# Kernel tuning notes

Hardware: AMD Instinct MI355X
Metric: run time of the kernel (lower is better)

The kernel has to match this reference:

```python
import jax, jax.numpy as jnp
import numpy as np

N_NODES = 50000
N_EDGES = 800000
D_IN, D_HID, D_OUT = 16, 64, 16
N_BLOCKS = 4


def setup_inputs() -> dict:
    key = jax.random.key(0)
    ks = jax.random.split(key, 12)
    s = 0.05  # small init scale to keep sum-aggregation over 4 blocks stable
    return {
        "x": jax.random.normal(ks[0], (N_NODES, D_IN), jnp.float32),
        "lframes": jax.random.normal(ks[1], (N_NODES, 4, 4), jnp.float32),
        "edge_index": jax.random.randint(ks[2], (2, N_EDGES), 0, N_NODES, jnp.int64),
        "lin_in_w": jax.random.normal(ks[3], (D_IN, D_HID), jnp.float32) * s,
        "lin_in_b": jnp.zeros((D_HID,), jnp.float32),
        # per-block mlp1: Linear(2D->D), ReLU, Linear(D->D), ReLU, Linear(D->D)
        "w0": jax.random.normal(ks[4], (N_BLOCKS, 2 * D_HID, D_HID), jnp.float32) * s,
        "b0": jnp.zeros((N_BLOCKS, D_HID), jnp.float32),
        "w1": jax.random.normal(ks[5], (N_BLOCKS, D_HID, D_HID), jnp.float32) * s,
        "b1": jnp.zeros((N_BLOCKS, D_HID), jnp.float32),
        "w2": jax.random.normal(ks[6], (N_BLOCKS, D_HID, D_HID), jnp.float32) * s,
        "b2": jnp.zeros((N_BLOCKS, D_HID), jnp.float32),
        "lin_out_w": jax.random.normal(ks[7], (D_HID, D_OUT), jnp.float32) * s,
        "lin_out_b": jnp.zeros((D_OUT,), jnp.float32),
    }


def reference(x, lframes, edge_index, lin_in_w, lin_in_b,
              w0, b0, w1, b1, w2, b2, lin_out_w, lin_out_b):
    src = edge_index[0]  # x_j (source / neighbor)
    dst = edge_index[1]  # x_i (target / aggregation node)
    h = x @ lin_in_w + lin_in_b  # [N, D]
    for k in range(N_BLOCKS):
        # message: cat((x_j, x_i)) -> mlp1 ; mlp2 is Identity (num_layers_mlp2=0)
        m = jnp.concatenate((h[src], h[dst]), axis=-1)  # [E, 2D]
        m = jax.nn.relu(m @ w0[k] + b0[k])
        m = jax.nn.relu(m @ w1[k] + b1[k])
        m = m @ w2[k] + b2[k]  # [E, D]
        # aggregate: scatter-add at target node
        h = jax.ops.segment_sum(m, dst, num_segments=N_NODES)
    return h @ lin_out_w + lin_out_b  # [N, D_OUT]
```

## Files before the change

kernel.cpp:

```cpp
#include <hip/hip_runtime.h>
#include <hip/hip_bf16.h>

#define N_NODES 50000
#define N_EDGES 800000
#define D_IN    16
#define D_HID   64
#define D_OUT   16
#define NCHUNK  ((N_NODES + 255) / 256)
#define TMAX    100352
#define GE8     ((N_EDGES / 8 + 255) / 256)
#define GH      ((N_NODES * D_HID + 255) / 256)
#define SCAP    48
#define NSLOTV  (N_NODES * SCAP / 8)

typedef __hip_bfloat16 bf16;
typedef _Float16 f16;
typedef _Float16 f16x8 __attribute__((ext_vector_type(8)));
typedef _Float16 f16x4 __attribute__((ext_vector_type(4)));
typedef float    f32x4 __attribute__((ext_vector_type(4)));
typedef _Float16 f16x8a __attribute__((ext_vector_type(8), may_alias));
typedef _Float16 f16x4a __attribute__((ext_vector_type(4), may_alias));
typedef int      i32x4 __attribute__((ext_vector_type(4)));
typedef unsigned short u16x8a __attribute__((ext_vector_type(8), may_alias));
typedef float    f32x4a __attribute__((ext_vector_type(4), may_alias));

__device__ __forceinline__ float b2f(bf16 v) { return __bfloat162float(v); }
__device__ __forceinline__ float bfb(unsigned short u) {
    union { unsigned u; float f; } z; z.u = (unsigned)u << 16; return z.f;
}
__device__ __forceinline__ int clampn(int v) {
    return v < 0 ? 0 : (v >= N_NODES ? N_NODES - 1 : v);
}
__device__ __forceinline__ float rdf(const void* p, long i, int isbf) {
    return isbf ? b2f(((const bf16*)p)[i]) : ((const float*)p)[i];
}
__device__ __forceinline__ f16x8 relu8(f16x8 v) {
#pragma unroll
    for (int j = 0; j < 8; j++) v[j] = v[j] > (f16)0 ? v[j] : (f16)0;
    return v;
}
__device__ __forceinline__ f16x4 relu4(f16x4 v) {
#pragma unroll
    for (int j = 0; j < 4; j++) v[j] = v[j] > (f16)0 ? v[j] : (f16)0;
    return v;
}
__device__ __forceinline__ int sbase(int m) {
    return (m & 0xFFFFF) * SCAP + ((m >> 25) & 3) * 16;
}

__global__ __launch_bounds__(256) void k_detect(const unsigned short* __restrict__ xw,
                                                const int* __restrict__ ei,
                                                int* __restrict__ flags,
                                                int* __restrict__ cursor,
                                                unsigned short* __restrict__ slots,
                                                unsigned short* __restrict__ psrc_us)
{
    int gtid = blockIdx.x * 256 + threadIdx.x;
    if (gtid < N_NODES) cursor[gtid] = 0;
    const int dpat = (int)0xC350C350;
    const i32x4 fillv = {dpat, dpat, dpat, dpat};
#pragma unroll
    for (int k = 0; k < 6; k++) {
        int q = k * (NCHUNK * 256) + gtid;
        if (q < NSLOTV) ((i32x4*)slots)[q] = fillv;
    }
    if (blockIdx.x == 0 && threadIdx.x < 64)
        psrc_us[(size_t)N_NODES * 64 + threadIdx.x] = 0xFC00u;
    if (blockIdx.x == 0 && threadIdx.x == 0) {
        int inband = 0;
        for (int j = 0; j < 256; j++) {
            unsigned short w = xw[2 * j];
            int e = (w >> 7) & 0xFF;
            if ((w & 0x7FFF) == 0 || (e >= 100 && e <= 140)) inband++;
        }
        flags[0] = (inband >= 192) ? 1 : 0;
        int z = 1;
        for (int j = 1; j < 128; j += 2) z &= (ei[j] == 0) ? 1 : 0;
        flags[1] = z;
    }
}

__global__ __launch_bounds__(256) void k_prep(const int* __restrict__ flags,
                                              const void* __restrict__ gw0,
                                              const void* __restrict__ gw1,
                                              const void* __restrict__ gw2,
                                              f16* __restrict__ wfrag,
                                              const int* __restrict__ eidx,
                                              int* __restrict__ cursor,
                                              unsigned short* __restrict__ slots,
                                              const void* __restrict__ x,
                                              const void* __restrict__ liw,
                                              const void* __restrict__ lib,
                                              float* __restrict__ h,
                                              const void* __restrict__ gb1,
                                              const void* __restrict__ gb2,
                                              float* __restrict__ cpad)
{
    const int isbf = flags[0];
    const int bid = blockIdx.x;
    if (bid < 32) {
        int idx = bid * 256 + threadIdx.x;
        int kb = idx >> 11, rem = idx & 2047;
        int slot = rem >> 6, lane = rem & 63;
        int lm = lane & 15, quad = lane >> 4;
        f16* outp = wfrag + (long)idx * 8;
        if (slot < 16) {
            int c = slot >> 2, q = slot & 3;
            long base = (long)kb * 2 * D_HID * D_HID;
#pragma unroll
            for (int j = 0; j < 8; j++)
                outp[j] = (f16)rdf(gw0, base + (long)(c * 32 + quad * 8 + j) * 64 + q * 16 + lm, isbf);
        } else {
            const void* gw = (slot < 24) ? gw1 : gw2;
            int s = (slot < 24) ? slot - 16 : slot - 24;
            int c = s >> 2, q = s & 3;
            long base = (long)kb * D_HID * D_HID;
#pragma unroll
            for (int j = 0; j < 8; j++)
                outp[j] = (f16)rdf(gw, base + (long)(c * 32 + quad * 8 + j) * 64 + q * 16 + lm, isbf);
        }
    } else if (bid < 32 + GE8) {
        int base = ((bid - 32) * 256 + threadIdx.x) * 8;
        if (base >= N_EDGES) return;
        const int strd = flags[1] ? 2 : 1;
        const long dbase = flags[1] ? (long)(2 * N_EDGES) : (long)N_EDGES;
        int d[8], s[8], pos[8], cnt = min(8, N_EDGES - base);
#pragma unroll
        for (int j = 0; j < 8; j++)
            if (j < cnt) {
                d[j] = clampn(eidx[dbase + (long)(base + j) * strd]);
                s[j] = clampn(eidx[(long)(base + j) * strd]);
            }
#pragma unroll
        for (int j = 0; j < 8; j++)
            if (j < cnt) pos[j] = atomicAdd(&cursor[d[j]], 1);
#pragma unroll
        for (int j = 0; j < 8; j++)
            if (j < cnt && pos[j] < SCAP)
                slots[d[j] * SCAP + pos[j]] = (unsigned short)s[j];
    } else if (bid < 32 + GE8 + GH) {
        int idx = (bid - 32 - GE8) * 256 + threadIdx.x;
        if (idx >= N_NODES * D_HID) return;
        int n = idx >> 6, c = idx & 63;
        float acc, wr[16], xr[16];
        if (isbf) {
            const unsigned short* xp = (const unsigned short*)x + (long)n * 16;
            u16x8a x0 = *(const u16x8a*)xp, x1 = *(const u16x8a*)(xp + 8);
#pragma unroll
            for (int i = 0; i < 8; i++) { xr[i] = bfb(x0[i]); xr[8 + i] = bfb(x1[i]); }
            const unsigned short* wq = (const unsigned short*)liw;
#pragma unroll
            for (int i = 0; i < 16; i++) wr[i] = bfb(wq[i * 64 + c]);
            acc = bfb(((const unsigned short*)lib)[c]);
        } else {
            const float* xp = (const float*)x + (long)n * 16;
#pragma unroll
            for (int q = 0; q < 4; q++) {
                f32x4a v = *(const f32x4a*)(xp + q * 4);
#pragma unroll
                for (int j = 0; j < 4; j++) xr[q * 4 + j] = v[j];
            }
            const float* wq = (const float*)liw;
#pragma unroll
            for (int i = 0; i < 16; i++) wr[i] = wq[i * 64 + c];
            acc = ((const float*)lib)[c];
        }
#pragma unroll
        for (int i = 0; i < 16; i++) acc += xr[i] * wr[i];
        h[idx] = acc;
    } else {
        int t = threadIdx.x;
        int k = t >> 6, j = t & 63;
        float acc = rdf(gb2, (long)k * 64 + j, isbf);
        for (int i = 0; i < 64; i++) {
            float zi = (float)(f16)fmaxf(rdf(gb1, (long)k * 64 + i, isbf), 0.f);
            float wi = (float)(f16)rdf(gw2, (long)k * 4096 + (long)i * 64 + j, isbf);
            acc += zi * wi;
        }
        cpad[k * 64 + j] = acc;
    }
}

__global__ __launch_bounds__(256) void k_scan1(const int* __restrict__ deg,
                                               int* __restrict__ bsum_t)
{
    __shared__ int rt[256];
    const int t = threadIdx.x;
    int i = blockIdx.x * 256 + t;
    int v = (i < N_NODES) ? deg[i] : 0;
    rt[t] = min((v + 15) >> 4, 3);
    __syncthreads();
    for (int d = 128; d > 0; d >>= 1) {
        if (t < d) rt[t] += rt[t + d];
        __syncthreads();
    }
    if (t == 0) bsum_t[blockIdx.x] = rt[0];
}

__global__ __launch_bounds__(256) void k_scan2(const int* __restrict__ bsum_t,
                                               int* __restrict__ boff_t,
                                               int* __restrict__ tot_t)
{
    __shared__ int st_[256];
    const int t = threadIdx.x;
    st_[t] = (t < NCHUNK) ? bsum_t[t] : 0;
    __syncthreads();
    for (int d = 1; d < 256; d <<= 1) {
        int vt = (t >= d) ? st_[t - d] : 0;
        __syncthreads();
        st_[t] += vt;
        __syncthreads();
    }
    if (t < NCHUNK) boff_t[t] = (t == 0) ? 0 : st_[t - 1];
    if (t == NCHUNK - 1) tot_t[0] = st_[t];
}

__global__ __launch_bounds__(256) void k_scan3(const int* __restrict__ deg,
                                               const int* __restrict__ boff_t,
                                               int* __restrict__ toff,
                                               int* __restrict__ tmeta)
{
    __shared__ int st_[256];
    const int t = threadIdx.x;
    int i = blockIdx.x * 256 + t;
    int v = (i < N_NODES) ? deg[i] : 0;
    int w = min((v + 15) >> 4, 3);
    st_[t] = w;
    __syncthreads();
    for (int d = 1; d < 256; d <<= 1) {
        int ut = (t >= d) ? st_[t - d] : 0;
        __syncthreads();
        st_[t] += ut;
        __syncthreads();
    }
    if (i < N_NODES) {
        int exT = boff_t[blockIdx.x] + st_[t] - w;
        toff[i] = exT;
        for (int j = 0; j < w; j++)
            tmeta[exT + j] = i | (min(16, v - 16 * j) << 20) | (j << 25);
    }
}

#define HP_ST 72

__global__ __launch_bounds__(256) void k_proj(
    const int* __restrict__ flags, float* hio,
    const f16* __restrict__ wfrag, const void* __restrict__ gb0,
    const int* __restrict__ deg,
    f16* __restrict__ psrc, f16* __restrict__ pdst, int kblk)
{
    __shared__ f16 hL_s[4][16 * HP_ST];

    const int tid  = threadIdx.x;
    const int isbf = flags[0];
    const int wv = tid >> 6, ln = tid & 63;
    const int lm = ln & 15, quad = ln >> 4;
    f16* hL = hL_s[wv];

    const int g = blockIdx.x * 4 + wv;
    if (g >= N_NODES / 16) return;
    const int n0 = g * 16;

    const f16* wb = wfrag + (long)kblk * 32 * 64 * 8;

#pragma unroll
    for (int i = 0; i < 16; i++) {
        int idx = i * 64 + ln;
        hL[(idx >> 6) * HP_ST + (idx & 63)] = (f16)hio[(long)n0 * 64 + idx];
    }
#pragma unroll
    for (int i = 0; i < 16; i++)
        if (deg[n0 + i] == 0) hio[(long)(n0 + i) * 64 + ln] = 0.f;

    f16x8 a[2];
#pragma unroll
    for (int c = 0; c < 2; c++)
        a[c] = *(const f16x8a*)&hL[lm * HP_ST + c * 32 + quad * 8];

    f32x4 accS[4], accD[4];
#pragma unroll
    for (int q = 0; q < 4; q++) {
        float bd = rdf(gb0, (long)kblk * 64 + q * 16 + lm, isbf);
        accS[q] = (f32x4){0.f, 0.f, 0.f, 0.f};
        accD[q] = (f32x4){bd, bd, bd, bd};
    }
#pragma unroll
    for (int c = 0; c < 2; c++)
#pragma unroll
        for (int q = 0; q < 4; q++) {
            f16x8 bs = *(const f16x8a*)&wb[(((c + 0) * 4 + q) * 64 + ln) * 8];
            f16x8 bd = *(const f16x8a*)&wb[(((c + 2) * 4 + q) * 64 + ln) * 8];
            accS[q] = __builtin_amdgcn_mfma_f32_16x16x32_f16(a[c], bs, accS[q], 0, 0, 0);
            accD[q] = __builtin_amdgcn_mfma_f32_16x16x32_f16(a[c], bd, accD[q], 0, 0, 0);
        }
#pragma unroll
    for (int q = 0; q < 4; q++)
#pragma unroll
        for (int r = 0; r < 4; r++) {
            long o = (long)(n0 + quad * 4 + r) * 64 + q * 16 + lm;
            psrc[o] = (f16)accS[q][r];
            pdst[o] = (f16)accD[q][r];
        }
}

#define Y_ST 72

__global__ __launch_bounds__(256) void k_edge_tile(
    const int* __restrict__ flags,
    const unsigned short* __restrict__ slots, const int* __restrict__ tmeta,
    const int* __restrict__ toff,
    const f16* __restrict__ psrc, const f16* __restrict__ pdst,
    float* __restrict__ hout,
    const f16* __restrict__ wfrag, const void* __restrict__ gb1,
    const void* __restrict__ gb2, const float* __restrict__ cpad, int kblk)
{
    __shared__ f16 y_s[4][16 * Y_ST];
    __shared__ float b1L[64], b2L[64], cpL[64];

    const int tid  = threadIdx.x;
    const int isbf = flags[0];
    const int wv = tid >> 6, ln = tid & 63;
    const int lm = ln & 15, quad = ln >> 4;
    const int sub = ln & 7, eh = ln >> 3;
    f16* y = y_s[wv];

    if (tid < 64)       b1L[tid]       = rdf(gb1, (long)kblk * 64 + tid, isbf);
    else if (tid < 128) b2L[tid - 64]  = rdf(gb2, (long)kblk * 64 + (tid - 64), isbf);
    else if (tid < 192) cpL[tid - 128] = cpad[kblk * 64 + (tid - 128)];
    __syncthreads();

    const f16* wb = wfrag + (long)kblk * 32 * 64 * 8;
    f16x8 bw1[2][4], bw2[2][4];
#pragma unroll
    for (int c = 0; c < 2; c++)
#pragma unroll
        for (int q = 0; q < 4; q++) {
            bw1[c][q] = *(const f16x8a*)&wb[((16 + c * 4 + q) * 64 + ln) * 8];
            bw2[c][q] = *(const f16x8a*)&wb[((24 + c * 4 + q) * 64 + ln) * 8];
        }

    const int T  = toff[N_NODES];
    const int W  = gridDim.x * 4;
    const int gw = blockIdx.x * 4 + wv;
    int t0 = (int)((long)gw * T / W);
    int t1 = (int)((long)(gw + 1) * T / W);
    if (t0 > 0)
        while (t0 < T && (tmeta[t0] & 0xFFFFF) == (tmeta[t0 - 1] & 0xFFFFF)) t0++;
    if (t1 > 0)
        while (t1 < T && (tmeta[t1] & 0xFFFFF) == (tmeta[t1 - 1] & 0xFFFFF)) t1++;
    if (t0 >= t1) return;

    int mA = tmeta[t0];
    int mB = tmeta[min(t0 + 1, T - 1)];
    int mC = tmeta[min(t0 + 2, T - 1)];
    int bA = sbase(mA), bB = sbase(mB);
    int sAa = slots[bA + eh], sAb = slots[bA + 8 + eh];
    int sBa = slots[bB + eh], sBb = slots[bB + 8 + eh];
    f16x8 psAa = *(const f16x8a*)&psrc[(long)sAa * 64 + sub * 8];
    f16x8 psAb = *(const f16x8a*)&psrc[(long)sAb * 64 + sub * 8];
    f16x8 pdA  = *(const f16x8a*)&pdst[(long)(mA & 0xFFFFF) * 64 + sub * 8];

    f32x4 accv[4];
#pragma unroll
    for (int q = 0; q < 4; q++) accv[q] = (f32x4){0.f, 0.f, 0.f, 0.f};

    for (int tt = t0; tt < t1; ++tt) {
        const int mD = tmeta[min(tt + 3, T - 1)];
        const int bC = sbase(mC);
        const int sCa = slots[bC + eh], sCb = slots[bC + 8 + eh];
        f16x8 psBa = *(const f16x8a*)&psrc[(long)sBa * 64 + sub * 8];
        f16x8 psBb = *(const f16x8a*)&psrc[(long)sBb * 64 + sub * 8];
        f16x8 pdB  = *(const f16x8a*)&pdst[(long)(mB & 0xFFFFF) * 64 + sub * 8];

        *(f16x8a*)&y[eh * Y_ST + sub * 8]       = relu8(psAa + pdA);
        *(f16x8a*)&y[(8 + eh) * Y_ST + sub * 8] = relu8(psAb + pdA);

        f16x8 a1[2];
        a1[0] = *(const f16x8a*)&y[lm * Y_ST + quad * 8];
        a1[1] = *(const f16x8a*)&y[lm * Y_ST + 32 + quad * 8];
        f32x4 acc1[4];
#pragma unroll
        for (int q = 0; q < 4; q++)
            acc1[q] = *(const f32x4a*)&b1L[q * 16 + quad * 4];
#pragma unroll
        for (int c = 0; c < 2; c++)
#pragma unroll
            for (int q = 0; q < 4; q++)
                acc1[q] = __builtin_amdgcn_mfma_f32_16x16x32_f16(bw1[c][q], a1[c], acc1[q], 0, 0, 0);
#pragma unroll
        for (int q = 0; q < 4; q++) {
            f16x4 pk = { (f16)acc1[q][0], (f16)acc1[q][1],
                         (f16)acc1[q][2], (f16)acc1[q][3] };
            *(f16x4a*)&y[lm * Y_ST + q * 16 + quad * 4] = relu4(pk);
        }

        f16x8 a2[2];
        a2[0] = *(const f16x8a*)&y[lm * Y_ST + quad * 8];
        a2[1] = *(const f16x8a*)&y[lm * Y_ST + 32 + quad * 8];
#pragma unroll
        for (int c = 0; c < 2; c++)
#pragma unroll
            for (int q = 0; q < 4; q++)
                accv[q] = __builtin_amdgcn_mfma_f32_16x16x32_f16(a2[c], bw2[c][q], accv[q], 0, 0, 0);

        const int curn = mA & 0xFFFFF;
        const int nxt  = (tt + 1 < t1) ? (mB & 0xFFFFF) : -1;
        if (nxt != curn) {
            const float npad = (float)(16 - ((mA >> 20) & 31));
            const float nt16 = (float)((((mA >> 25) & 3) + 1) * 16);
#pragma unroll
            for (int q = 0; q < 4; q++) {
                float v = accv[q][0] + accv[q][1] + accv[q][2] + accv[q][3];
                v += __shfl_xor(v, 16, 64);
                v += __shfl_xor(v, 32, 64);
                if (quad == 0) {
                    const int f = q * 16 + lm;
                    hout[(long)curn * 64 + f] = v + nt16 * b2L[f] - npad * cpL[f];
                }
                accv[q] = (f32x4){0.f, 0.f, 0.f, 0.f};
            }
        }

        mA = mB; mB = mC; mC = mD;
        sBa = sCa; sBb = sCb;
        psAa = psBa; psAb = psBb; pdA = pdB;
    }
}

__global__ __launch_bounds__(256) void k_lin_out(const int* __restrict__ flags,
                                                 const float* __restrict__ h,
                                                 const void* __restrict__ w,
                                                 const void* __restrict__ b,
                                                 float* __restrict__ out)
{
    __shared__ float wl[D_HID * D_OUT];
    __shared__ float bl[D_OUT];
    const int isbf = flags[0];
    const int t = threadIdx.x;
    for (int k = t; k < D_HID * D_OUT; k += 256) wl[k] = rdf(w, k, isbf);
    if (t < D_OUT) bl[t] = rdf(b, t, isbf);
    __syncthreads();

    int idx = blockIdx.x * 256 + t;
    if (idx >= N_NODES * D_OUT) return;
    int n = idx >> 4, c = idx & 15;
    const float* hr = h + (long)n * D_HID;
    float acc = bl[c];
#pragma unroll
    for (int i = 0; i < 16; i++) {
        f32x4a v = *(const f32x4a*)(hr + i * 4);
        acc += v[0] * wl[(i * 4 + 0) * 16 + c] + v[1] * wl[(i * 4 + 1) * 16 + c]
             + v[2] * wl[(i * 4 + 2) * 16 + c] + v[3] * wl[(i * 4 + 3) * 16 + c];
    }
    out[idx] = acc;
}

extern "C" void kernel_launch(void* const* d_in, const int* in_sizes, int n_in,
                              void* d_out, int out_size, void* d_ws, size_t ws_size,
                              hipStream_t stream)
{
    const void* x    = d_in[0];
    const int*  ei   = (const int*)d_in[2];
    const void* liw  = d_in[3];
    const void* lib  = d_in[4];
    const void* w0   = d_in[5];
    const void* b0   = d_in[6];
    const void* w1   = d_in[7];
    const void* b1   = d_in[8];
    const void* w2   = d_in[9];
    const void* b2   = d_in[10];
    const void* low  = d_in[11];
    const void* lob  = d_in[12];
    float* out = (float*)d_out;

    char* wp = (char*)d_ws;
    int*   flags  = (int*)wp;                 wp += 256;
    float* hA     = (float*)wp;               wp += (size_t)N_NODES * D_HID * 4;
    f16*   Psrc   = (f16*)wp;                 wp += ((size_t)N_NODES + 1) * D_HID * 2;
    f16*   Pdst   = (f16*)wp;                 wp += (size_t)N_NODES * D_HID * 2;
    f16*   wfrag  = (f16*)wp;                 wp += (size_t)4 * 32 * 64 * 8 * 2;
    float* cpad   = (float*)wp;               wp += (size_t)4 * 64 * 4;
    int*   cursor = (int*)wp;                 wp += (size_t)N_NODES * 4;
    int*   bsum_t = (int*)wp;                 wp += 256 * 4;
    int*   boff_t = (int*)wp;                 wp += 256 * 4;
    int*   tmeta  = (int*)wp;                 wp += (size_t)TMAX * 4;
    unsigned short* slots = (unsigned short*)wp; wp += (size_t)N_NODES * SCAP * 2;
    int*   toff   = (int*)wp;

    k_detect<<<NCHUNK, 256, 0, stream>>>((const unsigned short*)x, ei, flags,
                                         cursor, slots, (unsigned short*)Psrc);
    k_prep<<<32 + GE8 + GH + 1, 256, 0, stream>>>(flags, w0, w1, w2, wfrag,
                                                  ei, cursor, slots,
                                                  x, liw, lib, hA, b1, b2, cpad);

    k_scan1<<<NCHUNK, 256, 0, stream>>>(cursor, bsum_t);
    k_scan2<<<1, 256, 0, stream>>>(bsum_t, boff_t, toff + N_NODES);
    k_scan3<<<NCHUNK, 256, 0, stream>>>(cursor, boff_t, toff, tmeta);

    for (int k = 0; k < 4; k++) {
        k_proj<<<(N_NODES / 16 + 3) / 4, 256, 0, stream>>>(flags, hA, wfrag, b0,
                                                           cursor, Psrc, Pdst, k);
        k_edge_tile<<<2048, 256, 0, stream>>>(flags, slots, tmeta, toff,
                                              Psrc, Pdst, hA, wfrag, b1, b2,
                                              cpad, k);
    }

    k_lin_out<<<(N_NODES * D_OUT + 255) / 256, 256, 0, stream>>>(flags, hA, low, lob, out);
}
```

Before: 397.0 us.

## Replace global per-node atomics with two-level bucketed CSR build in LDS

Edge slot construction is now two-level. Edges are first binned into coarse buckets of 512 destination nodes using block-local LDS counters and one global atomic per bucket. A new per-bucket kernel then builds the per-node slot lists in shared memory and writes them out along with the degrees and tile counts. This replaces per-edge global atomics on cursors, the full global slot pre-fill and the separate scan1 kernel. In exchange it adds an intermediate bucket buffer with a fixed capacity per bucket (BCAP) that could overflow on skewed inputs, and the bucket kernel runs on only 98 blocks.

```diff
diff --git a/kernel.cpp b/kernel.cpp
--- a/kernel.cpp
+++ b/kernel.cpp
@@ -11,7 +11,8 @@
 #define GE8     ((N_EDGES / 8 + 255) / 256)
 #define GH      ((N_NODES * D_HID + 255) / 256)
 #define SCAP    48
-#define NSLOTV  (N_NODES * SCAP / 8)
+#define NB      98
+#define BCAP    12288
 
 typedef __hip_bfloat16 bf16;
 typedef _Float16 f16;
@@ -20,7 +21,6 @@
 typedef float    f32x4 __attribute__((ext_vector_type(4)));
 typedef _Float16 f16x8a __attribute__((ext_vector_type(8), may_alias));
 typedef _Float16 f16x4a __attribute__((ext_vector_type(4), may_alias));
-typedef int      i32x4 __attribute__((ext_vector_type(4)));
 typedef unsigned short u16x8a __attribute__((ext_vector_type(8), may_alias));
 typedef float    f32x4a __attribute__((ext_vector_type(4), may_alias));
 
@@ -51,22 +51,13 @@
 __global__ __launch_bounds__(256) void k_detect(const unsigned short* __restrict__ xw,
                                                 const int* __restrict__ ei,
                                                 int* __restrict__ flags,
-                                                int* __restrict__ cursor,
-                                                unsigned short* __restrict__ slots,
+                                                int* __restrict__ gbcnt,
                                                 unsigned short* __restrict__ psrc_us)
 {
-    int gtid = blockIdx.x * 256 + threadIdx.x;
-    if (gtid < N_NODES) cursor[gtid] = 0;
-    const int dpat = (int)0xC350C350;
-    const i32x4 fillv = {dpat, dpat, dpat, dpat};
-#pragma unroll
-    for (int k = 0; k < 6; k++) {
-        int q = k * (NCHUNK * 256) + gtid;
-        if (q < NSLOTV) ((i32x4*)slots)[q] = fillv;
-    }
-    if (blockIdx.x == 0 && threadIdx.x < 64)
-        psrc_us[(size_t)N_NODES * 64 + threadIdx.x] = 0xFC00u;
-    if (blockIdx.x == 0 && threadIdx.x == 0) {
+    const int t = threadIdx.x;
+    if (t < 64) psrc_us[(size_t)N_NODES * 64 + t] = 0xFC00u;
+    if (t < NB) gbcnt[t] = 0;
+    if (t == 0) {
         int inband = 0;
         for (int j = 0; j < 256; j++) {
             unsigned short w = xw[2 * j];
@@ -86,8 +77,8 @@
                                               const void* __restrict__ gw2,
                                               f16* __restrict__ wfrag,
                                               const int* __restrict__ eidx,
-                                              int* __restrict__ cursor,
-                                              unsigned short* __restrict__ slots,
+                                              int* __restrict__ gbcnt,
+                                              unsigned int* __restrict__ gbuckets,
                                               const void* __restrict__ x,
                                               const void* __restrict__ liw,
                                               const void* __restrict__ lib,
@@ -120,24 +111,37 @@
                 outp[j] = (f16)rdf(gw, base + (long)(c * 32 + quad * 8 + j) * 64 + q * 16 + lm, isbf);
         }
     } else if (bid < 32 + GE8) {
-        int base = ((bid - 32) * 256 + threadIdx.x) * 8;
-        if (base >= N_EDGES) return;
+        __shared__ int cnt[NB], base[NB];
+        const int t = threadIdx.x;
+        for (int k = t; k < NB; k += 256) cnt[k] = 0;
+        __syncthreads();
+        const int ebase = ((bid - 32) * 256 + t) * 8;
+        const int cntv = (ebase < N_EDGES) ? min(8, N_EDGES - ebase) : 0;
         const int strd = flags[1] ? 2 : 1;
         const long dbase = flags[1] ? (long)(2 * N_EDGES) : (long)N_EDGES;
-        int d[8], s[8], pos[8], cnt = min(8, N_EDGES - base);
+        int d[8], s[8], r[8];
 #pragma unroll
         for (int j = 0; j < 8; j++)
-            if (j < cnt) {
-                d[j] = clampn(eidx[dbase + (long)(base + j) * strd]);
-                s[j] = clampn(eidx[(long)(base + j) * strd]);
+            if (j < cntv) {
+                d[j] = clampn(eidx[dbase + (long)(ebase + j) * strd]);
+                s[j] = clampn(eidx[(long)(ebase + j) * strd]);
             }
 #pragma unroll
         for (int j = 0; j < 8; j++)
-            if (j < cnt) pos[j] = atomicAdd(&cursor[d[j]], 1);
+            if (j < cntv) r[j] = atomicAdd(&cnt[d[j] >> 9], 1);
+        __syncthreads();
+        for (int k = t; k < NB; k += 256)
+            base[k] = cnt[k] ? atomicAdd(&gbcnt[k], cnt[k]) : 0;
+        __syncthreads();
 #pragma unroll
         for (int j = 0; j < 8; j++)
-            if (j < cnt && pos[j] < SCAP)
-                slots[d[j] * SCAP + pos[j]] = (unsigned short)s[j];
+            if (j < cntv) {
+                int b = d[j] >> 9;
+                int p = base[b] + r[j];
+                if (p < BCAP)
+                    gbuckets[(size_t)b * BCAP + p] =
+                        ((unsigned)(d[j] & 511) << 16) | (unsigned)s[j];
+            }
     } else if (bid < 32 + GE8 + GH) {
         int idx = (bid - 32 - GE8) * 256 + threadIdx.x;
         if (idx >= N_NODES * D_HID) return;
@@ -181,20 +185,50 @@
     }
 }
 
-__global__ __launch_bounds__(256) void k_scan1(const int* __restrict__ deg,
-                                               int* __restrict__ bsum_t)
-{
-    __shared__ int rt[256];
-    const int t = threadIdx.x;
-    int i = blockIdx.x * 256 + t;
-    int v = (i < N_NODES) ? deg[i] : 0;
-    rt[t] = min((v + 15) >> 4, 3);
+__global__ __launch_bounds__(256) void k_bucket(const int* __restrict__ gbcnt,
+                                                const unsigned int* __restrict__ gbuckets,
+                                                unsigned short* __restrict__ slots,
+                                                int* __restrict__ deg,
+                                                int* __restrict__ bsum_t)
+{
+    __shared__ unsigned short sl[512 * SCAP];
+    __shared__ int cur[512];
+    __shared__ int red[256];
+    const int t = threadIdx.x, b = blockIdx.x;
+
+    for (int k = t; k < 512; k += 256) cur[k] = 0;
+    unsigned int* sl32 = (unsigned int*)sl;
+    for (int k = t; k < 512 * SCAP / 2; k += 256) sl32[k] = 0xC350C350u;
     __syncthreads();
-    for (int d = 128; d > 0; d >>= 1) {
-        if (t < d) rt[t] += rt[t + d];
-        __syncthreads();
-    }
-    if (t == 0) bsum_t[blockIdx.x] = rt[0];
+
+    const int ne = min(gbcnt[b], BCAP);
+    const unsigned int* eb = gbuckets + (size_t)b * BCAP;
+    for (int k = t; k < ne; k += 256) {
+        unsigned int rec = eb[k];
+        int n = rec >> 16;
+        int pos = atomicAdd(&cur[n], 1);
+        if (pos < SCAP) sl[n * SCAP + pos] = (unsigned short)(rec & 0xFFFFu);
+    }
+    __syncthreads();
+
+    const int n0 = b * 512;
+    const int nn = min(512, N_NODES - n0);
+    unsigned int* gs32 = (unsigned int*)slots;
+    for (int k = t; k < nn * SCAP / 2; k += 256)
+        gs32[(size_t)n0 * SCAP / 2 + k] = sl32[k];
+    for (int half = 0; half < 2; half++) {
+        int n = half * 256 + t;
+        int dv = (n < nn) ? cur[n] : 0;
+        if (n < nn) deg[n0 + n] = dv;
+        red[t] = min((dv + 15) >> 4, 3);
+        __syncthreads();
+        for (int d2 = 128; d2 > 0; d2 >>= 1) {
+            if (t < d2) red[t] += red[t + d2];
+            __syncthreads();
+        }
+        if (t == 0) bsum_t[b * 2 + half] = red[0];
+        __syncthreads();
+    }
 }
 
 __global__ __launch_bounds__(256) void k_scan2(const int* __restrict__ bsum_t,
@@ -485,15 +519,17 @@
     int*   boff_t = (int*)wp;                 wp += 256 * 4;
     int*   tmeta  = (int*)wp;                 wp += (size_t)TMAX * 4;
     unsigned short* slots = (unsigned short*)wp; wp += (size_t)N_NODES * SCAP * 2;
-    int*   toff   = (int*)wp;
-
-    k_detect<<<NCHUNK, 256, 0, stream>>>((const unsigned short*)x, ei, flags,
-                                         cursor, slots, (unsigned short*)Psrc);
+    int*   toff   = (int*)wp;                 wp += ((size_t)N_NODES + 4) * 4;
+    int*   gbcnt  = (int*)wp;                 wp += 128 * 4;
+    unsigned int* gbuckets = (unsigned int*)wp;
+
+    k_detect<<<1, 256, 0, stream>>>((const unsigned short*)x, ei, flags,
+                                    gbcnt, (unsigned short*)Psrc);
     k_prep<<<32 + GE8 + GH + 1, 256, 0, stream>>>(flags, w0, w1, w2, wfrag,
-                                                  ei, cursor, slots,
+                                                  ei, gbcnt, gbuckets,
                                                   x, liw, lib, hA, b1, b2, cpad);
-
-    k_scan1<<<NCHUNK, 256, 0, stream>>>(cursor, bsum_t);
+    k_bucket<<<NB, 256, 0, stream>>>(gbcnt, gbuckets, slots, cursor, bsum_t);
+
     k_scan2<<<1, 256, 0, stream>>>(bsum_t, boff_t, toff + N_NODES);
     k_scan3<<<NCHUNK, 256, 0, stream>>>(cursor, boff_t, toff, tmeta);
 
```

New measurement: 396.2 us. No clear change (-0.2%).
